# Kernel tuning notes

Measured on AMD Instinct MI355X. Metric: run time of the kernel, lower is better.

Reference implementation:

```python
import jax, jax.numpy as jnp
import numpy as np

N = 50000      # num nodes
E = 20000      # num hyperedges
NNZ = 800000   # incidence entries
F_IN = 256
HID = [256, 256]
EPS = 1e-5     # BatchNorm eps


def setup_inputs() -> dict:
    key = jax.random.key(0)
    ks = jax.random.split(key, 12)
    x = jax.random.normal(ks[0], (N, F_IN), jnp.float32)
    node_idx = jax.random.randint(ks[1], (NNZ,), 0, N, dtype=jnp.int32)
    edge_idx = jax.random.randint(ks[2], (NNZ,), 0, E, dtype=jnp.int32)
    hyperedge_index = jnp.stack([node_idx, edge_idx])  # [2, NNZ]
    hyperedge_weight = jax.random.uniform(ks[3], (E,), jnp.float32, 0.1, 1.0)
    # layer params: Linear(in, out, bias) + BatchNorm(gamma, beta)
    W1 = jax.random.normal(ks[4], (F_IN, HID[0]), jnp.float32) * (1.0 / np.sqrt(F_IN))
    b1 = jax.random.normal(ks[5], (HID[0],), jnp.float32) * 0.02
    g1 = jnp.ones((HID[0],), jnp.float32)
    be1 = jnp.zeros((HID[0],), jnp.float32)
    W2 = jax.random.normal(ks[6], (HID[0], HID[1]), jnp.float32) * (1.0 / np.sqrt(HID[0]))
    b2 = jax.random.normal(ks[7], (HID[1],), jnp.float32) * 0.02
    g2 = jnp.ones((HID[1],), jnp.float32)
    be2 = jnp.zeros((HID[1],), jnp.float32)
    return dict(x=x, hyperedge_index=hyperedge_index, hyperedge_weight=hyperedge_weight,
                W1=W1, b1=b1, g1=g1, be1=be1, W2=W2, b2=b2, g2=g2, be2=be2)


def _hypergraph_layer(x, node_idx, edge_idx, w_e, W, b, g, be):
    """One HypergraphLayer: HypergraphConv (no attention, heads=1) + BN(train) + ReLU.

    PyG HypergraphConv math: out = D^{-1} H B^{-1} H^T (X Theta) + bias,
    where D_i = sum of incident hyperedge weights, B_e = hyperedge cardinality.
    """
    x = x @ W                                   # [N, F_out] node transform
    # node degree weighted by hyperedge weight
    D = jax.ops.segment_sum(w_e[edge_idx], node_idx, num_segments=N)
    Dinv = jnp.where(D != 0, 1.0 / D, 0.0)
    # hyperedge cardinality
    B = jax.ops.segment_sum(jnp.ones((NNZ,), x.dtype), edge_idx, num_segments=E)
    Binv = jnp.where(B != 0, 1.0 / B, 0.0)
    # node -> edge aggregation: e = B^{-1} H^T x
    e = Binv[:, None] * jax.ops.segment_sum(x[node_idx], edge_idx, num_segments=E)
    # edge -> node aggregation: out = D^{-1} H e
    out = Dinv[:, None] * jax.ops.segment_sum(e[edge_idx], node_idx, num_segments=N)
    out = out + b
    # BatchNorm1d (training mode: biased batch stats over the node dim)
    mu = out.mean(axis=0)
    var = out.var(axis=0)
    out = (out - mu) * jax.lax.rsqrt(var + EPS) * g + be
    return jax.nn.relu(out)                     # dropout p=0.0 -> identity


def reference(x, hyperedge_index, hyperedge_weight, W1, b1, g1, be1, W2, b2, g2, be2):
    node_idx = hyperedge_index[0]
    edge_idx = hyperedge_index[1]
    h = _hypergraph_layer(x, node_idx, edge_idx, hyperedge_weight, W1, b1, g1, be1)
    h = _hypergraph_layer(h, node_idx, edge_idx, hyperedge_weight, W2, b2, g2, be2)
    return h
```

## Files before the change

kernel.cpp:

```cpp
#include <hip/hip_runtime.h>

#define NN     50000
#define NE     20000
#define NNZV   800000
#define FD     256
#define EPSV   1e-5f
#define MPAD   20032
#define NCPY   128
#define EPB    (NNZV / NCPY)
#define HEC    (NE / 2)
#define HNC    (NN / 2)
#define HTC    (HEC + HNC)
#define BE     ((NE + 255) / 256)
#define BN     ((NN + 255) / 256)

typedef __attribute__((ext_vector_type(8))) __bf16 bf16x8;
typedef __attribute__((ext_vector_type(4))) __bf16 bf16x4;
typedef __attribute__((ext_vector_type(4))) float f32x4;

__device__ __forceinline__ float b2f(unsigned short u) {
  union { unsigned int i; float f; } z; z.i = ((unsigned)u) << 16; return z.f;
}


__global__ __launch_bounds__(256) void
hg_histlds(const int* __restrict__ nidx, const int* __restrict__ eidx,
           unsigned* __restrict__ cntc,
           unsigned short* __restrict__ rank_e16, unsigned short* __restrict__ rank_n16) {
  __shared__ unsigned hist[HTC];
  int b = blockIdx.x, t = threadIdx.x;
  for (int j = t; j < HTC; j += 256) hist[j] = 0;
  __syncthreads();
  int i0 = b * EPB;
  for (int i = i0 + t; i < i0 + EPB; i += 256) {
    int e = eidx[i];
    int n = nidx[i];
    unsigned se = (e & 1) * 16;
    unsigned sn = (n & 1) * 16;
    unsigned oe = atomicAdd(&hist[e >> 1], 1u << se);
    unsigned on = atomicAdd(&hist[HEC + (n >> 1)], 1u << sn);
    rank_e16[i] = (unsigned short)((oe >> se) & 0xffffu);
    rank_n16[i] = (unsigned short)((on >> sn) & 0xffffu);
  }
  __syncthreads();
  unsigned* dst = cntc + (size_t)b * HTC;
  for (int j = t; j < HTC; j += 256) dst[j] = hist[j];
}

__global__ void hg_colreduce(unsigned* __restrict__ cntc,
                             int* __restrict__ total_e, int* __restrict__ total_n) {
  int j = blockIdx.x * 256 + threadIdx.x;
  if (j >= HTC) return;
  unsigned run = 0;
#pragma unroll 4
  for (int c = 0; c < NCPY; ++c) {
    unsigned v = cntc[(size_t)c * HTC + j];
    cntc[(size_t)c * HTC + j] = run;
    run += v;
  }
  if (j < HEC) {
    total_e[2 * j]     = run & 0xffffu;
    total_e[2 * j + 1] = run >> 16;
  } else {
    int k = j - HEC;
    total_n[2 * k]     = run & 0xffffu;
    total_n[2 * k + 1] = run >> 16;
  }
}


__global__ void hg_scan1(const int* __restrict__ total_e, const int* __restrict__ total_n,
                         int* __restrict__ part) {
  __shared__ int lds[256];
  int b = blockIdx.x;
  const int* src;
  int n, idx0;
  if (b < BE) { src = total_e; n = NE; idx0 = b * 256; }
  else        { src = total_n; n = NN; idx0 = (b - BE) * 256; }
  int t = threadIdx.x;
  int idx = idx0 + t;
  lds[t] = (idx < n) ? src[idx] : 0;
  for (int d = 128; d > 0; d >>= 1) {
    __syncthreads();
    if (t < d) lds[t] += lds[t + d];
  }
  if (t == 0) part[b] = lds[0];
}

__global__ void hg_scan2(int* __restrict__ part, int* __restrict__ off_e,
                         int* __restrict__ off_n) {
  __shared__ int lds[256];
  int t = threadIdx.x;
  int v = (t < BE) ? part[t] : 0;
  lds[t] = v;
  for (int d = 1; d < 256; d <<= 1) {
    __syncthreads();
    int u = (t >= d) ? lds[t - d] : 0;
    int w = lds[t];
    __syncthreads();
    lds[t] = u + w;
  }
  __syncthreads();
  if (t < BE) part[t] = lds[t] - v;
  if (t == 255) off_e[NE] = lds[255];
  __syncthreads();
  v = (t < BN) ? part[BE + t] : 0;
  lds[t] = v;
  for (int d = 1; d < 256; d <<= 1) {
    __syncthreads();
    int u = (t >= d) ? lds[t - d] : 0;
    int w = lds[t];
    __syncthreads();
    lds[t] = u + w;
  }
  __syncthreads();
  if (t < BN) part[BE + t] = lds[t] - v;
  if (t == 255) off_n[NN] = lds[255];
}

__global__ void hg_scan3(const int* __restrict__ total_e, const int* __restrict__ total_n,
                         const int* __restrict__ part,
                         int* __restrict__ off_e, int* __restrict__ off_n) {
  __shared__ int lds[256];
  int b = blockIdx.x;
  const int* src;
  int* dst;
  int n, idx0;
  if (b < BE) { src = total_e; dst = off_e; n = NE; idx0 = b * 256; }
  else        { src = total_n; dst = off_n; n = NN; idx0 = (b - BE) * 256; }
  int base = part[b];
  int t = threadIdx.x;
  int idx = idx0 + t;
  int v = (idx < n) ? src[idx] : 0;
  lds[t] = v;
  for (int d = 1; d < 256; d <<= 1) {
    __syncthreads();
    int u = (t >= d) ? lds[t - d] : 0;
    int w = lds[t];
    __syncthreads();
    lds[t] = u + w;
  }
  __syncthreads();
  if (idx < n) dst[idx] = base + lds[t] - v;
}


__global__ void hg_scatter(const int* __restrict__ nidx, const int* __restrict__ eidx,
                           const unsigned* __restrict__ cntc,
                           const unsigned short* __restrict__ rank_e16,
                           const unsigned short* __restrict__ rank_n16,
                           const int* __restrict__ off_e, const int* __restrict__ off_n,
                           int* __restrict__ mem_e, int* __restrict__ mem_n) {
  int i = blockIdx.x * 256 + threadIdx.x;
  if (i >= NNZV) return;
  unsigned copy = (unsigned)i / EPB;
  int e = eidx[i];
  int n = nidx[i];
  unsigned be = cntc[(size_t)copy * HTC + (e >> 1)];
  be = (be >> ((e & 1) * 16)) & 0xffffu;
  unsigned bn = cntc[(size_t)copy * HTC + HEC + (n >> 1)];
  bn = (bn >> ((n & 1) * 16)) & 0xffffu;
  mem_e[off_e[e] + be + rank_e16[i]] = n;
  mem_n[off_n[n] + bn + rank_n16[i]] = e;
}


__global__ void hg_prep(const float* __restrict__ W1, const float* __restrict__ W2,
                        __bf16* __restrict__ Wt1, __bf16* __restrict__ Wt2,
                        const float* __restrict__ X, __bf16* __restrict__ Xbf) {
  int bid = blockIdx.x;
  if (bid < FD) {
    int id = bid * 256 + threadIdx.x;
    int n = id >> 8;
    int k = id & 255;
    Wt1[n * FD + k] = (__bf16)W1[k * FD + n];
    Wt2[n * FD + k] = (__bf16)W2[k * FD + n];
  } else {
    int idx = (bid - FD) * 256 + threadIdx.x;
    if (idx < NN * FD / 4) {
      float4 v = ((const float4*)X)[idx];
      bf16x4 o = {(__bf16)v.x, (__bf16)v.y, (__bf16)v.z, (__bf16)v.w};
      ((bf16x4*)Xbf)[idx] = o;
    }
  }
}


template<int APPLY>
__global__ __launch_bounds__(256) void
hg_agg_n2e_bf(const __bf16* __restrict__ Xbf, const int* __restrict__ off_e,
              const int* __restrict__ mem_e,
              const float* __restrict__ scale, const float* __restrict__ shift,
              __bf16* __restrict__ Ebf) {
  int wid = blockIdx.x * 4 + (threadIdx.x >> 6);
  if (wid >= NE) return;
  int lane = threadIdx.x & 63;
  int c = lane * 4;
  float4 sc = {0.f, 0.f, 0.f, 0.f}, sh = {0.f, 0.f, 0.f, 0.f};
  if (APPLY) {
    sc = *(const float4*)(scale + c);
    sh = *(const float4*)(shift + c);
  }
  const unsigned short* Xu = (const unsigned short*)Xbf;
  int lo = off_e[wid], hi = off_e[wid + 1];
  float a0 = 0.f, a1 = 0.f, a2 = 0.f, a3 = 0.f;

#define ACC4(v) do { \
    float f0 = b2f((v).x), f1 = b2f((v).y), f2 = b2f((v).z), f3 = b2f((v).w); \
    if (APPLY) { \
      f0 = fmaxf(fmaf(f0, sc.x, sh.x), 0.f); \
      f1 = fmaxf(fmaf(f1, sc.y, sh.y), 0.f); \
      f2 = fmaxf(fmaf(f2, sc.z, sh.z), 0.f); \
      f3 = fmaxf(fmaf(f3, sc.w, sh.w), 0.f); \
    } \
    a0 += f0; a1 += f1; a2 += f2; a3 += f3; } while (0)

  int m = lo;
  for (; m + 8 <= hi; m += 8) {
    int i0 = mem_e[m],     i1 = mem_e[m + 1], i2 = mem_e[m + 2], i3 = mem_e[m + 3];
    int i4 = mem_e[m + 4], i5 = mem_e[m + 5], i6 = mem_e[m + 6], i7 = mem_e[m + 7];
    ushort4 v0 = *(const ushort4*)(Xu + (size_t)i0 * FD + c);
    ushort4 v1 = *(const ushort4*)(Xu + (size_t)i1 * FD + c);
    ushort4 v2 = *(const ushort4*)(Xu + (size_t)i2 * FD + c);
    ushort4 v3 = *(const ushort4*)(Xu + (size_t)i3 * FD + c);
    ushort4 v4 = *(const ushort4*)(Xu + (size_t)i4 * FD + c);
    ushort4 v5 = *(const ushort4*)(Xu + (size_t)i5 * FD + c);
    ushort4 v6 = *(const ushort4*)(Xu + (size_t)i6 * FD + c);
    ushort4 v7 = *(const ushort4*)(Xu + (size_t)i7 * FD + c);
    ACC4(v0); ACC4(v1); ACC4(v2); ACC4(v3);
    ACC4(v4); ACC4(v5); ACC4(v6); ACC4(v7);
  }
  for (; m + 4 <= hi; m += 4) {
    int i0 = mem_e[m], i1 = mem_e[m + 1], i2 = mem_e[m + 2], i3 = mem_e[m + 3];
    ushort4 v0 = *(const ushort4*)(Xu + (size_t)i0 * FD + c);
    ushort4 v1 = *(const ushort4*)(Xu + (size_t)i1 * FD + c);
    ushort4 v2 = *(const ushort4*)(Xu + (size_t)i2 * FD + c);
    ushort4 v3 = *(const ushort4*)(Xu + (size_t)i3 * FD + c);
    ACC4(v0); ACC4(v1); ACC4(v2); ACC4(v3);
  }
  for (; m < hi; ++m) {
    int i0 = mem_e[m];
    ushort4 v0 = *(const ushort4*)(Xu + (size_t)i0 * FD + c);
    ACC4(v0);
  }
  int cnt = hi - lo;
  float bi = cnt ? 1.0f / (float)cnt : 0.0f;
  bf16x4 o = {(__bf16)(a0 * bi), (__bf16)(a1 * bi), (__bf16)(a2 * bi), (__bf16)(a3 * bi)};
  *(bf16x4*)(Ebf + (size_t)wid * FD + c) = o;
}


__global__ __launch_bounds__(256) void
hg_gemm(const __bf16* __restrict__ A, const __bf16* __restrict__ Bt,
        __bf16* __restrict__ C, int Mrows) {
  int w = threadIdx.x >> 6, l = threadIdx.x & 63;
  int m0 = blockIdx.x * 64 + w * 16;
  int n0 = blockIdx.y * 64;
  int kb = (l >> 4) * 8;
  const bf16x8* Ap = (const bf16x8*)(A + (size_t)(m0 + (l & 15)) * FD + kb);
  const __bf16* Bbase = Bt + (size_t)(n0 + (l & 15)) * FD + kb;
  f32x4 acc0 = {0.f, 0.f, 0.f, 0.f}, acc1 = {0.f, 0.f, 0.f, 0.f};
  f32x4 acc2 = {0.f, 0.f, 0.f, 0.f}, acc3 = {0.f, 0.f, 0.f, 0.f};
#pragma unroll
  for (int ks = 0; ks < 8; ++ks) {
    bf16x8 a = Ap[ks * 4];
    bf16x8 b0 = *(const bf16x8*)(Bbase + (size_t)( 0) * FD + ks * 32);
    bf16x8 b1 = *(const bf16x8*)(Bbase + (size_t)(16) * FD + ks * 32);
    bf16x8 b2 = *(const bf16x8*)(Bbase + (size_t)(32) * FD + ks * 32);
    bf16x8 b3 = *(const bf16x8*)(Bbase + (size_t)(48) * FD + ks * 32);
    acc0 = __builtin_amdgcn_mfma_f32_16x16x32_bf16(a, b0, acc0, 0, 0, 0);
    acc1 = __builtin_amdgcn_mfma_f32_16x16x32_bf16(a, b1, acc1, 0, 0, 0);
    acc2 = __builtin_amdgcn_mfma_f32_16x16x32_bf16(a, b2, acc2, 0, 0, 0);
    acc3 = __builtin_amdgcn_mfma_f32_16x16x32_bf16(a, b3, acc3, 0, 0, 0);
  }
  int crow = m0 + (l >> 4) * 4;
  int ccol = n0 + (l & 15);
#pragma unroll
  for (int r = 0; r < 4; ++r) {
    int rr = crow + r;
    if (rr < Mrows) {
      C[(size_t)rr * FD + ccol +  0] = (__bf16)acc0[r];
      C[(size_t)rr * FD + ccol + 16] = (__bf16)acc1[r];
      C[(size_t)rr * FD + ccol + 32] = (__bf16)acc2[r];
      C[(size_t)rr * FD + ccol + 48] = (__bf16)acc3[r];
    }
  }
}


__global__ __launch_bounds__(256) void
hg_agg_e2n_bf(const __bf16* __restrict__ eWbf, const int* __restrict__ off_n,
              const int* __restrict__ mem_n, const float* __restrict__ wedge,
              const float* __restrict__ bias, __bf16* __restrict__ Outbf) {
  int node = blockIdx.x * 4 + (threadIdx.x >> 6);
  if (node >= NN) return;
  int lane = threadIdx.x & 63;
  int c = lane * 4;
  const unsigned short* eWu = (const unsigned short*)eWbf;
  int lo = off_n[node], hi = off_n[node + 1];
  float a0 = 0.f, a1 = 0.f, a2 = 0.f, a3 = 0.f;
  float dw = 0.f;
  int m = lo;
  for (; m + 8 <= hi; m += 8) {
    int i0 = mem_n[m],     i1 = mem_n[m + 1], i2 = mem_n[m + 2], i3 = mem_n[m + 3];
    int i4 = mem_n[m + 4], i5 = mem_n[m + 5], i6 = mem_n[m + 6], i7 = mem_n[m + 7];
    ushort4 v0 = *(const ushort4*)(eWu + (size_t)i0 * FD + c);
    ushort4 v1 = *(const ushort4*)(eWu + (size_t)i1 * FD + c);
    ushort4 v2 = *(const ushort4*)(eWu + (size_t)i2 * FD + c);
    ushort4 v3 = *(const ushort4*)(eWu + (size_t)i3 * FD + c);
    ushort4 v4 = *(const ushort4*)(eWu + (size_t)i4 * FD + c);
    ushort4 v5 = *(const ushort4*)(eWu + (size_t)i5 * FD + c);
    ushort4 v6 = *(const ushort4*)(eWu + (size_t)i6 * FD + c);
    ushort4 v7 = *(const ushort4*)(eWu + (size_t)i7 * FD + c);
    dw += wedge[i0] + wedge[i1] + wedge[i2] + wedge[i3]
        + wedge[i4] + wedge[i5] + wedge[i6] + wedge[i7];
    a0 += b2f(v0.x); a1 += b2f(v0.y); a2 += b2f(v0.z); a3 += b2f(v0.w);
    a0 += b2f(v1.x); a1 += b2f(v1.y); a2 += b2f(v1.z); a3 += b2f(v1.w);
    a0 += b2f(v2.x); a1 += b2f(v2.y); a2 += b2f(v2.z); a3 += b2f(v2.w);
    a0 += b2f(v3.x); a1 += b2f(v3.y); a2 += b2f(v3.z); a3 += b2f(v3.w);
    a0 += b2f(v4.x); a1 += b2f(v4.y); a2 += b2f(v4.z); a3 += b2f(v4.w);
    a0 += b2f(v5.x); a1 += b2f(v5.y); a2 += b2f(v5.z); a3 += b2f(v5.w);
    a0 += b2f(v6.x); a1 += b2f(v6.y); a2 += b2f(v6.z); a3 += b2f(v6.w);
    a0 += b2f(v7.x); a1 += b2f(v7.y); a2 += b2f(v7.z); a3 += b2f(v7.w);
  }
  for (; m < hi; ++m) {
    int i0 = mem_n[m];
    ushort4 v0 = *(const ushort4*)(eWu + (size_t)i0 * FD + c);
    dw += wedge[i0];
    a0 += b2f(v0.x); a1 += b2f(v0.y); a2 += b2f(v0.z); a3 += b2f(v0.w);
  }
  float di = (dw != 0.f) ? 1.0f / dw : 0.0f;
  float4 b4 = *(const float4*)(bias + c);
  bf16x4 o = {(__bf16)fmaf(a0, di, b4.x), (__bf16)fmaf(a1, di, b4.y),
              (__bf16)fmaf(a2, di, b4.z), (__bf16)fmaf(a3, di, b4.w)};
  *(bf16x4*)(Outbf + (size_t)node * FD + c) = o;
}


__global__ __launch_bounds__(256) void
hg_stats(const __bf16* __restrict__ Outbf, float* __restrict__ stats) {
  int c = threadIdx.x;
  int rpb = (NN + gridDim.x - 1) / gridDim.x;
  int r0 = blockIdx.x * rpb;
  int r1 = r0 + rpb;
  if (r1 > NN) r1 = NN;
  const unsigned short* Ou = (const unsigned short*)Outbf;
  float s = 0.f, q = 0.f;
  for (int r = r0; r < r1; ++r) {
    float v = b2f(Ou[(size_t)r * FD + c]);
    s += v;
    q = fmaf(v, v, q);
  }
  atomicAdd(&stats[c], s);
  atomicAdd(&stats[FD + c], q);
}


__global__ void hg_bn_finalize(const float* __restrict__ stats, const float* __restrict__ g,
                               const float* __restrict__ be,
                               float* __restrict__ scale, float* __restrict__ shift) {
  int c = threadIdx.x;
  float mu = stats[c] * (1.0f / NN);
  float var = stats[FD + c] * (1.0f / NN) - mu * mu;
  float sc = g[c] * rsqrtf(var + EPSV);
  scale[c] = sc;
  shift[c] = fmaf(-mu, sc, be[c]);
}

__global__ void hg_apply_bf(const __bf16* __restrict__ Outbf, const float* __restrict__ scale,
                            const float* __restrict__ shift, float* __restrict__ H) {
  int idx = blockIdx.x * 256 + threadIdx.x;
  if (idx >= NN * FD / 8) return;
  ushort4 v0 = ((const ushort4*)Outbf)[idx * 2 + 0];
  ushort4 v1 = ((const ushort4*)Outbf)[idx * 2 + 1];
  int c = (idx & (FD / 8 - 1)) * 8;
  float4 sa = *(const float4*)(scale + c);
  float4 sb = *(const float4*)(scale + c + 4);
  float4 ha = *(const float4*)(shift + c);
  float4 hb = *(const float4*)(shift + c + 4);
  float4 o0, o1;
  o0.x = fmaxf(fmaf(b2f(v0.x), sa.x, ha.x), 0.f);
  o0.y = fmaxf(fmaf(b2f(v0.y), sa.y, ha.y), 0.f);
  o0.z = fmaxf(fmaf(b2f(v0.z), sa.z, ha.z), 0.f);
  o0.w = fmaxf(fmaf(b2f(v0.w), sa.w, ha.w), 0.f);
  o1.x = fmaxf(fmaf(b2f(v1.x), sb.x, hb.x), 0.f);
  o1.y = fmaxf(fmaf(b2f(v1.y), sb.y, hb.y), 0.f);
  o1.z = fmaxf(fmaf(b2f(v1.z), sb.z, hb.z), 0.f);
  o1.w = fmaxf(fmaf(b2f(v1.w), sb.w, hb.w), 0.f);
  ((float4*)H)[idx * 2 + 0] = o0;
  ((float4*)H)[idx * 2 + 1] = o1;
}


extern "C" void kernel_launch(void* const* d_in, const int* in_sizes, int n_in,
                              void* d_out, int out_size, void* d_ws, size_t ws_size,
                              hipStream_t stream) {
  const float* x    = (const float*)d_in[0];
  const int*   hei  = (const int*)d_in[1];
  const int*   nidx = hei;
  const int*   eidx = hei + NNZV;
  const float* wedge = (const float*)d_in[2];
  const float* W1  = (const float*)d_in[3];
  const float* b1  = (const float*)d_in[4];
  const float* g1  = (const float*)d_in[5];
  const float* be1 = (const float*)d_in[6];
  const float* W2  = (const float*)d_in[7];
  const float* b2  = (const float*)d_in[8];
  const float* g2  = (const float*)d_in[9];
  const float* be2 = (const float*)d_in[10];
  float* out = (float*)d_out;

  char* base = (char*)d_ws;
  size_t cur = 0;
  auto alloc = [&](size_t bytes) -> void* {
    void* p = base + cur;
    cur += (bytes + 255) & ~(size_t)255;
    return p;
  };
  unsigned* cntc = (unsigned*)alloc((size_t)NCPY * HTC * 4);
  unsigned short* rank_e16 = (unsigned short*)alloc((size_t)NNZV * 2);
  unsigned short* rank_n16 = (unsigned short*)alloc((size_t)NNZV * 2);
  int*   total_e = (int*)alloc(NE * 4);
  int*   total_n = (int*)alloc(NN * 4);
  int*   part  = (int*)alloc((BE + BN) * 4);
  int*   off_e = (int*)alloc((NE + 1) * 4);
  int*   off_n = (int*)alloc((NN + 1) * 4);
  int*   mem_e = (int*)alloc((size_t)NNZV * 4);
  int*   mem_n = (int*)alloc((size_t)NNZV * 4);
  __bf16* Wt1  = (__bf16*)alloc(FD * FD * 2);
  __bf16* Wt2  = (__bf16*)alloc(FD * FD * 2);
  __bf16* Xbf  = (__bf16*)alloc((size_t)NN * FD * 2);
  __bf16* Ebf  = (__bf16*)alloc((size_t)MPAD * FD * 2);
  __bf16* eWbf = (__bf16*)alloc((size_t)MPAD * FD * 2);
  __bf16* Outbf = (__bf16*)alloc((size_t)NN * FD * 2);
  float* stats = (float*)alloc(2 * FD * 4);
  float* scale1 = (float*)alloc(FD * 4);
  float* shift1 = (float*)alloc(FD * 4);
  float* scale2 = (float*)alloc(FD * 4);
  float* shift2 = (float*)alloc(FD * 4);
  if (cur > ws_size) return;

  hg_histlds<<<NCPY, 256, 0, stream>>>(nidx, eidx, cntc, rank_e16, rank_n16);
  hg_colreduce<<<(HTC + 255) / 256, 256, 0, stream>>>(cntc, total_e, total_n);
  hg_scan1<<<BE + BN, 256, 0, stream>>>(total_e, total_n, part);
  hg_scan2<<<1, 256, 0, stream>>>(part, off_e, off_n);
  hg_scan3<<<BE + BN, 256, 0, stream>>>(total_e, total_n, part, off_e, off_n);
  hg_scatter<<<(NNZV + 255) / 256, 256, 0, stream>>>(nidx, eidx, cntc, rank_e16, rank_n16,
                                                     off_e, off_n, mem_e, mem_n);
  hg_prep<<<FD + (NN * FD / 4 + 255) / 256, 256, 0, stream>>>(W1, W2, Wt1, Wt2, x, Xbf);

  const int N2E_BLOCKS = (NE + 3) / 4;
  const int E2N_BLOCKS = (NN + 3) / 4;
  const dim3 GEMM_GRID(MPAD / 64, 4);

  hg_agg_n2e_bf<0><<<N2E_BLOCKS, 256, 0, stream>>>(Xbf, off_e, mem_e, nullptr, nullptr, Ebf);
  hg_gemm<<<GEMM_GRID, 256, 0, stream>>>(Ebf, Wt1, eWbf, NE);
  hg_agg_e2n_bf<<<E2N_BLOCKS, 256, 0, stream>>>(eWbf, off_n, mem_n, wedge, b1, Outbf);
  hipMemsetAsync(stats, 0, 2 * FD * 4, stream);
  hg_stats<<<256, 256, 0, stream>>>(Outbf, stats);
  hg_bn_finalize<<<1, FD, 0, stream>>>(stats, g1, be1, scale1, shift1);

  hg_agg_n2e_bf<1><<<N2E_BLOCKS, 256, 0, stream>>>(Outbf, off_e, mem_e, scale1, shift1, Ebf);
  hg_gemm<<<GEMM_GRID, 256, 0, stream>>>(Ebf, Wt2, eWbf, NE);
  hg_agg_e2n_bf<<<E2N_BLOCKS, 256, 0, stream>>>(eWbf, off_n, mem_n, wedge, b2, Outbf);
  hipMemsetAsync(stats, 0, 2 * FD * 4, stream);
  hg_stats<<<256, 256, 0, stream>>>(Outbf, stats);
  hg_bn_finalize<<<1, FD, 0, stream>>>(stats, g2, be2, scale2, shift2);
  hg_apply_bf<<<(NN * FD / 8 + 255) / 256, 256, 0, stream>>>(Outbf, scale2, shift2, out);
}
```

Before: 589.4 us.

## Store node and edge features in column-panel layout for gather locality

Node features are now stored as 32-column panels (panel-major, row within panel) and the GEMM writes edge features as 64-column panels. Both gather kernels loop over the panels one at a time, with lanes split between several neighbours and a few columns, then combine partial sums by shuffles. The aim is a smaller working set per pass so gathered rows stay in L2/MALL, at the cost of more gather instructions, shuffle reductions and masked-lane waste on low-degree rows.

```diff
diff --git a/kernel.cpp b/kernel.cpp
--- a/kernel.cpp
+++ b/kernel.cpp
@@ -167,7 +167,7 @@
 
 __global__ void hg_prep(const float* __restrict__ W1, const float* __restrict__ W2,
                         __bf16* __restrict__ Wt1, __bf16* __restrict__ Wt2,
-                        const float* __restrict__ X, __bf16* __restrict__ Xbf) {
+                        const float* __restrict__ X, __bf16* __restrict__ Xp) {
   int bid = blockIdx.x;
   if (bid < FD) {
     int id = bid * 256 + threadIdx.x;
@@ -177,10 +177,12 @@
     Wt2[n * FD + k] = (__bf16)W2[k * FD + n];
   } else {
     int idx = (bid - FD) * 256 + threadIdx.x;
-    if (idx < NN * FD / 4) {
-      float4 v = ((const float4*)X)[idx];
+    if (idx < NN * 64) {
+      int r = idx >> 6;
+      int c = (idx & 63) * 4;
+      float4 v = *(const float4*)(X + (size_t)r * FD + c);
       bf16x4 o = {(__bf16)v.x, (__bf16)v.y, (__bf16)v.z, (__bf16)v.w};
-      ((bf16x4*)Xbf)[idx] = o;
+      *(bf16x4*)(Xp + (size_t)(c >> 5) * NN * 32 + (size_t)r * 32 + (c & 31)) = o;
     }
   }
 }
@@ -188,71 +190,69 @@
 
 template<int APPLY>
 __global__ __launch_bounds__(256) void
-hg_agg_n2e_bf(const __bf16* __restrict__ Xbf, const int* __restrict__ off_e,
-              const int* __restrict__ mem_e,
-              const float* __restrict__ scale, const float* __restrict__ shift,
-              __bf16* __restrict__ Ebf) {
+hg_agg_n2e_p(const __bf16* __restrict__ Xp, const int* __restrict__ off_e,
+             const int* __restrict__ mem_e,
+             const float* __restrict__ scale, const float* __restrict__ shift,
+             __bf16* __restrict__ Ebf) {
   int wid = blockIdx.x * 4 + (threadIdx.x >> 6);
   if (wid >= NE) return;
-  int lane = threadIdx.x & 63;
-  int c = lane * 4;
-  float4 sc = {0.f, 0.f, 0.f, 0.f}, sh = {0.f, 0.f, 0.f, 0.f};
-  if (APPLY) {
-    sc = *(const float4*)(scale + c);
-    sh = *(const float4*)(shift + c);
-  }
-  const unsigned short* Xu = (const unsigned short*)Xbf;
+  int l = threadIdx.x & 63;
+  int g = l >> 3;
+  int cq = l & 7;
   int lo = off_e[wid], hi = off_e[wid + 1];
-  float a0 = 0.f, a1 = 0.f, a2 = 0.f, a3 = 0.f;
-
-#define ACC4(v) do { \
-    float f0 = b2f((v).x), f1 = b2f((v).y), f2 = b2f((v).z), f3 = b2f((v).w); \
-    if (APPLY) { \
-      f0 = fmaxf(fmaf(f0, sc.x, sh.x), 0.f); \
-      f1 = fmaxf(fmaf(f1, sc.y, sh.y), 0.f); \
-      f2 = fmaxf(fmaf(f2, sc.z, sh.z), 0.f); \
-      f3 = fmaxf(fmaf(f3, sc.w, sh.w), 0.f); \
-    } \
-    a0 += f0; a1 += f1; a2 += f2; a3 += f3; } while (0)
-
-  int m = lo;
-  for (; m + 8 <= hi; m += 8) {
-    int i0 = mem_e[m],     i1 = mem_e[m + 1], i2 = mem_e[m + 2], i3 = mem_e[m + 3];
-    int i4 = mem_e[m + 4], i5 = mem_e[m + 5], i6 = mem_e[m + 6], i7 = mem_e[m + 7];
-    ushort4 v0 = *(const ushort4*)(Xu + (size_t)i0 * FD + c);
-    ushort4 v1 = *(const ushort4*)(Xu + (size_t)i1 * FD + c);
-    ushort4 v2 = *(const ushort4*)(Xu + (size_t)i2 * FD + c);
-    ushort4 v3 = *(const ushort4*)(Xu + (size_t)i3 * FD + c);
-    ushort4 v4 = *(const ushort4*)(Xu + (size_t)i4 * FD + c);
-    ushort4 v5 = *(const ushort4*)(Xu + (size_t)i5 * FD + c);
-    ushort4 v6 = *(const ushort4*)(Xu + (size_t)i6 * FD + c);
-    ushort4 v7 = *(const ushort4*)(Xu + (size_t)i7 * FD + c);
-    ACC4(v0); ACC4(v1); ACC4(v2); ACC4(v3);
-    ACC4(v4); ACC4(v5); ACC4(v6); ACC4(v7);
-  }
-  for (; m + 4 <= hi; m += 4) {
-    int i0 = mem_e[m], i1 = mem_e[m + 1], i2 = mem_e[m + 2], i3 = mem_e[m + 3];
-    ushort4 v0 = *(const ushort4*)(Xu + (size_t)i0 * FD + c);
-    ushort4 v1 = *(const ushort4*)(Xu + (size_t)i1 * FD + c);
-    ushort4 v2 = *(const ushort4*)(Xu + (size_t)i2 * FD + c);
-    ushort4 v3 = *(const ushort4*)(Xu + (size_t)i3 * FD + c);
-    ACC4(v0); ACC4(v1); ACC4(v2); ACC4(v3);
-  }
-  for (; m < hi; ++m) {
-    int i0 = mem_e[m];
-    ushort4 v0 = *(const ushort4*)(Xu + (size_t)i0 * FD + c);
-    ACC4(v0);
-  }
   int cnt = hi - lo;
   float bi = cnt ? 1.0f / (float)cnt : 0.0f;
-  bf16x4 o = {(__bf16)(a0 * bi), (__bf16)(a1 * bi), (__bf16)(a2 * bi), (__bf16)(a3 * bi)};
-  *(bf16x4*)(Ebf + (size_t)wid * FD + c) = o;
+  const unsigned short* memu = (const unsigned short*)mem_e;
+  (void)memu;
+#pragma unroll 1
+  for (int p = 0; p < 8; ++p) {
+    int cbase = p * 32 + cq * 4;
+    float4 sc = {0.f,0.f,0.f,0.f}, sh = {0.f,0.f,0.f,0.f};
+    if (APPLY) {
+      sc = *(const float4*)(scale + cbase);
+      sh = *(const float4*)(shift + cbase);
+    }
+    const unsigned short* base = (const unsigned short*)Xp + (size_t)p * NN * 32 + cq * 4;
+    float a0 = 0.f, a1 = 0.f, a2 = 0.f, a3 = 0.f;
+#define N2E_ACC(v, live) do { \
+      float f0 = b2f((v).x), f1 = b2f((v).y), f2 = b2f((v).z), f3 = b2f((v).w); \
+      if (APPLY) { \
+        f0 = fmaxf(fmaf(f0, sc.x, sh.x), 0.f); \
+        f1 = fmaxf(fmaf(f1, sc.y, sh.y), 0.f); \
+        f2 = fmaxf(fmaf(f2, sc.z, sh.z), 0.f); \
+        f3 = fmaxf(fmaf(f3, sc.w, sh.w), 0.f); \
+      } \
+      if (live) { a0 += f0; a1 += f1; a2 += f2; a3 += f3; } } while (0)
+    for (int m = lo; m < hi; m += 32) {
+      int mA = m + g, mB = m + 8 + g, mC = m + 16 + g, mD = m + 24 + g;
+      int iA = mem_e[min(mA, hi - 1)];
+      int iB = mem_e[min(mB, hi - 1)];
+      int iC = mem_e[min(mC, hi - 1)];
+      int iD = mem_e[min(mD, hi - 1)];
+      ushort4 vA = *(const ushort4*)(base + (size_t)iA * 32);
+      ushort4 vB = *(const ushort4*)(base + (size_t)iB * 32);
+      ushort4 vC = *(const ushort4*)(base + (size_t)iC * 32);
+      ushort4 vD = *(const ushort4*)(base + (size_t)iD * 32);
+      N2E_ACC(vA, mA < hi); N2E_ACC(vB, mB < hi);
+      N2E_ACC(vC, mC < hi); N2E_ACC(vD, mD < hi);
+    }
+    a0 += __shfl_xor(a0, 8);  a1 += __shfl_xor(a1, 8);
+    a2 += __shfl_xor(a2, 8);  a3 += __shfl_xor(a3, 8);
+    a0 += __shfl_xor(a0, 16); a1 += __shfl_xor(a1, 16);
+    a2 += __shfl_xor(a2, 16); a3 += __shfl_xor(a3, 16);
+    a0 += __shfl_xor(a0, 32); a1 += __shfl_xor(a1, 32);
+    a2 += __shfl_xor(a2, 32); a3 += __shfl_xor(a3, 32);
+    if (g == 0) {
+      bf16x4 o = {(__bf16)(a0 * bi), (__bf16)(a1 * bi), (__bf16)(a2 * bi), (__bf16)(a3 * bi)};
+      *(bf16x4*)(Ebf + (size_t)wid * FD + cbase) = o;
+    }
+  }
 }
 
 
 __global__ __launch_bounds__(256) void
 hg_gemm(const __bf16* __restrict__ A, const __bf16* __restrict__ Bt,
-        __bf16* __restrict__ C, int Mrows) {
+        __bf16* __restrict__ Cp, int Mrows) {
   int w = threadIdx.x >> 6, l = threadIdx.x & 63;
   int m0 = blockIdx.x * 64 + w * 16;
   int n0 = blockIdx.y * 64;
@@ -274,80 +274,92 @@
     acc3 = __builtin_amdgcn_mfma_f32_16x16x32_bf16(a, b3, acc3, 0, 0, 0);
   }
   int crow = m0 + (l >> 4) * 4;
-  int ccol = n0 + (l & 15);
+  int lc = l & 15;
+  __bf16* P = Cp + (size_t)blockIdx.y * MPAD * 64;
 #pragma unroll
   for (int r = 0; r < 4; ++r) {
     int rr = crow + r;
     if (rr < Mrows) {
-      C[(size_t)rr * FD + ccol +  0] = (__bf16)acc0[r];
-      C[(size_t)rr * FD + ccol + 16] = (__bf16)acc1[r];
-      C[(size_t)rr * FD + ccol + 32] = (__bf16)acc2[r];
-      C[(size_t)rr * FD + ccol + 48] = (__bf16)acc3[r];
+      P[(size_t)rr * 64 + lc +  0] = (__bf16)acc0[r];
+      P[(size_t)rr * 64 + lc + 16] = (__bf16)acc1[r];
+      P[(size_t)rr * 64 + lc + 32] = (__bf16)acc2[r];
+      P[(size_t)rr * 64 + lc + 48] = (__bf16)acc3[r];
     }
   }
 }
 
 
 __global__ __launch_bounds__(256) void
-hg_agg_e2n_bf(const __bf16* __restrict__ eWbf, const int* __restrict__ off_n,
-              const int* __restrict__ mem_n, const float* __restrict__ wedge,
-              const float* __restrict__ bias, __bf16* __restrict__ Outbf) {
+hg_agg_e2n_p(const __bf16* __restrict__ eWp, const int* __restrict__ off_n,
+             const int* __restrict__ mem_n, const float* __restrict__ wedge,
+             const float* __restrict__ bias, __bf16* __restrict__ Outp) {
   int node = blockIdx.x * 4 + (threadIdx.x >> 6);
   if (node >= NN) return;
-  int lane = threadIdx.x & 63;
-  int c = lane * 4;
-  const unsigned short* eWu = (const unsigned short*)eWbf;
+  int l = threadIdx.x & 63;
+  int g = l >> 4;
+  int cq = l & 15;
   int lo = off_n[node], hi = off_n[node + 1];
-  float a0 = 0.f, a1 = 0.f, a2 = 0.f, a3 = 0.f;
-  float dw = 0.f;
-  int m = lo;
-  for (; m + 8 <= hi; m += 8) {
-    int i0 = mem_n[m],     i1 = mem_n[m + 1], i2 = mem_n[m + 2], i3 = mem_n[m + 3];
-    int i4 = mem_n[m + 4], i5 = mem_n[m + 5], i6 = mem_n[m + 6], i7 = mem_n[m + 7];
-    ushort4 v0 = *(const ushort4*)(eWu + (size_t)i0 * FD + c);
-    ushort4 v1 = *(const ushort4*)(eWu + (size_t)i1 * FD + c);
-    ushort4 v2 = *(const ushort4*)(eWu + (size_t)i2 * FD + c);
-    ushort4 v3 = *(const ushort4*)(eWu + (size_t)i3 * FD + c);
-    ushort4 v4 = *(const ushort4*)(eWu + (size_t)i4 * FD + c);
-    ushort4 v5 = *(const ushort4*)(eWu + (size_t)i5 * FD + c);
-    ushort4 v6 = *(const ushort4*)(eWu + (size_t)i6 * FD + c);
-    ushort4 v7 = *(const ushort4*)(eWu + (size_t)i7 * FD + c);
-    dw += wedge[i0] + wedge[i1] + wedge[i2] + wedge[i3]
-        + wedge[i4] + wedge[i5] + wedge[i6] + wedge[i7];
-    a0 += b2f(v0.x); a1 += b2f(v0.y); a2 += b2f(v0.z); a3 += b2f(v0.w);
-    a0 += b2f(v1.x); a1 += b2f(v1.y); a2 += b2f(v1.z); a3 += b2f(v1.w);
-    a0 += b2f(v2.x); a1 += b2f(v2.y); a2 += b2f(v2.z); a3 += b2f(v2.w);
-    a0 += b2f(v3.x); a1 += b2f(v3.y); a2 += b2f(v3.z); a3 += b2f(v3.w);
-    a0 += b2f(v4.x); a1 += b2f(v4.y); a2 += b2f(v4.z); a3 += b2f(v4.w);
-    a0 += b2f(v5.x); a1 += b2f(v5.y); a2 += b2f(v5.z); a3 += b2f(v5.w);
-    a0 += b2f(v6.x); a1 += b2f(v6.y); a2 += b2f(v6.z); a3 += b2f(v6.w);
-    a0 += b2f(v7.x); a1 += b2f(v7.y); a2 += b2f(v7.z); a3 += b2f(v7.w);
-  }
-  for (; m < hi; ++m) {
-    int i0 = mem_n[m];
-    ushort4 v0 = *(const ushort4*)(eWu + (size_t)i0 * FD + c);
-    dw += wedge[i0];
-    a0 += b2f(v0.x); a1 += b2f(v0.y); a2 += b2f(v0.z); a3 += b2f(v0.w);
-  }
-  float di = (dw != 0.f) ? 1.0f / dw : 0.0f;
-  float4 b4 = *(const float4*)(bias + c);
-  bf16x4 o = {(__bf16)fmaf(a0, di, b4.x), (__bf16)fmaf(a1, di, b4.y),
-              (__bf16)fmaf(a2, di, b4.z), (__bf16)fmaf(a3, di, b4.w)};
-  *(bf16x4*)(Outbf + (size_t)node * FD + c) = o;
+  float di = 0.f;
+#pragma unroll 1
+  for (int p = 0; p < 4; ++p) {
+    const unsigned short* base = (const unsigned short*)eWp + (size_t)p * MPAD * 64 + cq * 4;
+    float a0 = 0.f, a1 = 0.f, a2 = 0.f, a3 = 0.f;
+    float dw = 0.f;
+    for (int m = lo; m < hi; m += 16) {
+      int mA = m + g, mB = m + 4 + g, mC = m + 8 + g, mD = m + 12 + g;
+      int iA = mem_n[min(mA, hi - 1)];
+      int iB = mem_n[min(mB, hi - 1)];
+      int iC = mem_n[min(mC, hi - 1)];
+      int iD = mem_n[min(mD, hi - 1)];
+      ushort4 vA = *(const ushort4*)(base + (size_t)iA * 64);
+      ushort4 vB = *(const ushort4*)(base + (size_t)iB * 64);
+      ushort4 vC = *(const ushort4*)(base + (size_t)iC * 64);
+      ushort4 vD = *(const ushort4*)(base + (size_t)iD * 64);
+      if (p == 0 && cq == 0) {
+        if (mA < hi) dw += wedge[iA];
+        if (mB < hi) dw += wedge[iB];
+        if (mC < hi) dw += wedge[iC];
+        if (mD < hi) dw += wedge[iD];
+      }
+      if (mA < hi) { a0 += b2f(vA.x); a1 += b2f(vA.y); a2 += b2f(vA.z); a3 += b2f(vA.w); }
+      if (mB < hi) { a0 += b2f(vB.x); a1 += b2f(vB.y); a2 += b2f(vB.z); a3 += b2f(vB.w); }
+      if (mC < hi) { a0 += b2f(vC.x); a1 += b2f(vC.y); a2 += b2f(vC.z); a3 += b2f(vC.w); }
+      if (mD < hi) { a0 += b2f(vD.x); a1 += b2f(vD.y); a2 += b2f(vD.z); a3 += b2f(vD.w); }
+    }
+    a0 += __shfl_xor(a0, 16); a1 += __shfl_xor(a1, 16);
+    a2 += __shfl_xor(a2, 16); a3 += __shfl_xor(a3, 16);
+    a0 += __shfl_xor(a0, 32); a1 += __shfl_xor(a1, 32);
+    a2 += __shfl_xor(a2, 32); a3 += __shfl_xor(a3, 32);
+    if (p == 0) {
+      dw += __shfl_xor(dw, 16);
+      dw += __shfl_xor(dw, 32);
+      dw = __shfl(dw, (threadIdx.x & 192));
+      di = (dw != 0.f) ? 1.0f / dw : 0.0f;
+    }
+    if (g == 0) {
+      int cbase = p * 64 + cq * 4;
+      float4 b4 = *(const float4*)(bias + cbase);
+      bf16x4 o = {(__bf16)fmaf(a0, di, b4.x), (__bf16)fmaf(a1, di, b4.y),
+                  (__bf16)fmaf(a2, di, b4.z), (__bf16)fmaf(a3, di, b4.w)};
+      *(bf16x4*)(Outp + (size_t)(cbase >> 5) * NN * 32 + (size_t)node * 32 + (cbase & 31)) = o;
+    }
+  }
 }
 
 
 __global__ __launch_bounds__(256) void
-hg_stats(const __bf16* __restrict__ Outbf, float* __restrict__ stats) {
-  int c = threadIdx.x;
+hg_stats(const __bf16* __restrict__ Outp, float* __restrict__ stats) {
+  int t = threadIdx.x;
+  int pnl = t >> 5, cc = t & 31;
+  int c = pnl * 32 + cc;
   int rpb = (NN + gridDim.x - 1) / gridDim.x;
   int r0 = blockIdx.x * rpb;
   int r1 = r0 + rpb;
   if (r1 > NN) r1 = NN;
-  const unsigned short* Ou = (const unsigned short*)Outbf;
+  const unsigned short* Ou = (const unsigned short*)Outp + (size_t)pnl * NN * 32 + cc;
   float s = 0.f, q = 0.f;
   for (int r = r0; r < r1; ++r) {
-    float v = b2f(Ou[(size_t)r * FD + c]);
+    float v = b2f(Ou[(size_t)r * 32]);
     s += v;
     q = fmaf(v, v, q);
   }
@@ -367,28 +379,22 @@
   shift[c] = fmaf(-mu, sc, be[c]);
 }
 
-__global__ void hg_apply_bf(const __bf16* __restrict__ Outbf, const float* __restrict__ scale,
+__global__ void hg_apply_bf(const __bf16* __restrict__ Outp, const float* __restrict__ scale,
                             const float* __restrict__ shift, float* __restrict__ H) {
   int idx = blockIdx.x * 256 + threadIdx.x;
-  if (idx >= NN * FD / 8) return;
-  ushort4 v0 = ((const ushort4*)Outbf)[idx * 2 + 0];
-  ushort4 v1 = ((const ushort4*)Outbf)[idx * 2 + 1];
-  int c = (idx & (FD / 8 - 1)) * 8;
+  if (idx >= NN * 64) return;
+  int r = idx >> 6;
+  int c = (idx & 63) * 4;
+  ushort4 v = *(const ushort4*)((const unsigned short*)Outp
+               + (size_t)(c >> 5) * NN * 32 + (size_t)r * 32 + (c & 31));
   float4 sa = *(const float4*)(scale + c);
-  float4 sb = *(const float4*)(scale + c + 4);
   float4 ha = *(const float4*)(shift + c);
-  float4 hb = *(const float4*)(shift + c + 4);
-  float4 o0, o1;
-  o0.x = fmaxf(fmaf(b2f(v0.x), sa.x, ha.x), 0.f);
-  o0.y = fmaxf(fmaf(b2f(v0.y), sa.y, ha.y), 0.f);
-  o0.z = fmaxf(fmaf(b2f(v0.z), sa.z, ha.z), 0.f);
-  o0.w = fmaxf(fmaf(b2f(v0.w), sa.w, ha.w), 0.f);
-  o1.x = fmaxf(fmaf(b2f(v1.x), sb.x, hb.x), 0.f);
-  o1.y = fmaxf(fmaf(b2f(v1.y), sb.y, hb.y), 0.f);
-  o1.z = fmaxf(fmaf(b2f(v1.z), sb.z, hb.z), 0.f);
-  o1.w = fmaxf(fmaf(b2f(v1.w), sb.w, hb.w), 0.f);
-  ((float4*)H)[idx * 2 + 0] = o0;
-  ((float4*)H)[idx * 2 + 1] = o1;
+  float4 o;
+  o.x = fmaxf(fmaf(b2f(v.x), sa.x, ha.x), 0.f);
+  o.y = fmaxf(fmaf(b2f(v.y), sa.y, ha.y), 0.f);
+  o.z = fmaxf(fmaf(b2f(v.z), sa.z, ha.z), 0.f);
+  o.w = fmaxf(fmaf(b2f(v.w), sa.w, ha.w), 0.f);
+  *(float4*)(H + (size_t)r * FD + c) = o;
 }
 
 
@@ -429,10 +435,10 @@
   int*   mem_n = (int*)alloc((size_t)NNZV * 4);
   __bf16* Wt1  = (__bf16*)alloc(FD * FD * 2);
   __bf16* Wt2  = (__bf16*)alloc(FD * FD * 2);
-  __bf16* Xbf  = (__bf16*)alloc((size_t)NN * FD * 2);
+  __bf16* Xp   = (__bf16*)alloc((size_t)NN * FD * 2);
   __bf16* Ebf  = (__bf16*)alloc((size_t)MPAD * FD * 2);
-  __bf16* eWbf = (__bf16*)alloc((size_t)MPAD * FD * 2);
-  __bf16* Outbf = (__bf16*)alloc((size_t)NN * FD * 2);
+  __bf16* eWp  = (__bf16*)alloc((size_t)MPAD * FD * 2);
+  __bf16* Outp = (__bf16*)alloc((size_t)NN * FD * 2);
   float* stats = (float*)alloc(2 * FD * 4);
   float* scale1 = (float*)alloc(FD * 4);
   float* shift1 = (float*)alloc(FD * 4);
@@ -447,24 +453,24 @@
   hg_scan3<<<BE + BN, 256, 0, stream>>>(total_e, total_n, part, off_e, off_n);
   hg_scatter<<<(NNZV + 255) / 256, 256, 0, stream>>>(nidx, eidx, cntc, rank_e16, rank_n16,
                                                      off_e, off_n, mem_e, mem_n);
-  hg_prep<<<FD + (NN * FD / 4 + 255) / 256, 256, 0, stream>>>(W1, W2, Wt1, Wt2, x, Xbf);
+  hg_prep<<<FD + (NN * 64 + 255) / 256, 256, 0, stream>>>(W1, W2, Wt1, Wt2, x, Xp);
 
   const int N2E_BLOCKS = (NE + 3) / 4;
   const int E2N_BLOCKS = (NN + 3) / 4;
   const dim3 GEMM_GRID(MPAD / 64, 4);
 
-  hg_agg_n2e_bf<0><<<N2E_BLOCKS, 256, 0, stream>>>(Xbf, off_e, mem_e, nullptr, nullptr, Ebf);
-  hg_gemm<<<GEMM_GRID, 256, 0, stream>>>(Ebf, Wt1, eWbf, NE);
-  hg_agg_e2n_bf<<<E2N_BLOCKS, 256, 0, stream>>>(eWbf, off_n, mem_n, wedge, b1, Outbf);
+  hg_agg_n2e_p<0><<<N2E_BLOCKS, 256, 0, stream>>>(Xp, off_e, mem_e, nullptr, nullptr, Ebf);
+  hg_gemm<<<GEMM_GRID, 256, 0, stream>>>(Ebf, Wt1, eWp, NE);
+  hg_agg_e2n_p<<<E2N_BLOCKS, 256, 0, stream>>>(eWp, off_n, mem_n, wedge, b1, Outp);
   hipMemsetAsync(stats, 0, 2 * FD * 4, stream);
-  hg_stats<<<256, 256, 0, stream>>>(Outbf, stats);
+  hg_stats<<<256, 256, 0, stream>>>(Outp, stats);
   hg_bn_finalize<<<1, FD, 0, stream>>>(stats, g1, be1, scale1, shift1);
 
-  hg_agg_n2e_bf<1><<<N2E_BLOCKS, 256, 0, stream>>>(Outbf, off_e, mem_e, scale1, shift1, Ebf);
-  hg_gemm<<<GEMM_GRID, 256, 0, stream>>>(Ebf, Wt2, eWbf, NE);
-  hg_agg_e2n_bf<<<E2N_BLOCKS, 256, 0, stream>>>(eWbf, off_n, mem_n, wedge, b2, Outbf);
+  hg_agg_n2e_p<1><<<N2E_BLOCKS, 256, 0, stream>>>(Outp, off_e, mem_e, scale1, shift1, Ebf);
+  hg_gemm<<<GEMM_GRID, 256, 0, stream>>>(Ebf, Wt2, eWp, NE);
+  hg_agg_e2n_p<<<E2N_BLOCKS, 256, 0, stream>>>(eWp, off_n, mem_n, wedge, b2, Outp);
   hipMemsetAsync(stats, 0, 2 * FD * 4, stream);
-  hg_stats<<<256, 256, 0, stream>>>(Outbf, stats);
+  hg_stats<<<256, 256, 0, stream>>>(Outp, stats);
   hg_bn_finalize<<<1, FD, 0, stream>>>(stats, g2, be2, scale2, shift2);
-  hg_apply_bf<<<(NN * FD / 8 + 255) / 256, 256, 0, stream>>>(Outbf, scale2, shift2, out);
-}
+  hg_apply_bf<<<(NN * 64 + 255) / 256, 256, 0, stream>>>(Outp, scale2, shift2, out);
+}
```

Result: slower. 672.8 us (+14.1%).
